# Performance work log

Hardware: AMD Instinct MI355X
Metric: run time of the kernel (lower is better)

The kernel has to match this reference:

```python
import jax, jax.numpy as jnp
import numpy as np
from jax import lax

B, S, PH, N = 4, 512, 4096, 16384
D, G, H, L, FF, GS = 1024, 128, 8, 4, 4096, 32
HD = D // H


def setup_inputs() -> dict:
    key = jax.random.key(0)
    ks = list(jax.random.split(key, 16))
    r = lambda k, sh: jax.random.normal(k, sh, jnp.float32) * 0.02
    return {
        'last_hidden': jax.random.normal(ks[0], (B, S, PH), jnp.float32),
        'current_pointcloud': jax.random.normal(ks[1], (B, N, 3), jnp.float32),
        'fp_w': r(ks[2], (D, PH)), 'fp_b': jnp.zeros((D,), jnp.float32),
        'sp_w': r(ks[3], (G * D, D)), 'sp_b': jnp.zeros((G * D,), jnp.float32),
        'pos_embed': r(ks[4], (1, G, D)),
        'ln1_w': jnp.ones((L, D), jnp.float32), 'ln1_b': jnp.zeros((L, D), jnp.float32),
        'in_w': r(ks[5], (L, 3 * D, D)), 'in_b': jnp.zeros((L, 3 * D), jnp.float32),
        'out_w': r(ks[6], (L, D, D)), 'out_b': jnp.zeros((L, D), jnp.float32),
        'ln2_w': jnp.ones((L, D), jnp.float32), 'ln2_b': jnp.zeros((L, D), jnp.float32),
        'mlp_w1': r(ks[7], (L, FF, D)), 'mlp_b1': jnp.zeros((L, FF), jnp.float32),
        'mlp_w2': r(ks[8], (L, D, FF)), 'mlp_b2': jnp.zeros((L, D), jnp.float32),
        'c1_w': r(ks[9], (D, D)), 'c1_b': jnp.zeros((D,), jnp.float32),
        'bn_g': jnp.ones((D,), jnp.float32), 'bn_beta': jnp.zeros((D,), jnp.float32),
        'bn_m': jnp.zeros((D,), jnp.float32), 'bn_v': jnp.ones((D,), jnp.float32),
        'c2_w': r(ks[10], (3 * GS, D)), 'c2_b': jnp.zeros((3 * GS,), jnp.float32),
    }


def _ln(x, w, b):
    m = jnp.mean(x, -1, keepdims=True)
    v = jnp.mean(jnp.square(x - m), -1, keepdims=True)
    return (x - m) * lax.rsqrt(v + 1e-5) * w + b


def _fps(xyz, num_samples):
    # iterative farthest point sampling; deterministic start index 0
    Bb, Nn, _ = xyz.shape
    dist0 = jnp.full((Bb, Nn), 1e10, xyz.dtype)
    far0 = jnp.zeros((Bb,), jnp.int32)

    def step(carry, _):
        dist, far = carry
        centroid = jnp.take_along_axis(xyz, far[:, None, None], axis=1)  # [B,1,3]
        d = jnp.sum(jnp.square(xyz - centroid), -1)                      # [B,N]
        dist = jnp.minimum(dist, d)
        return (dist, jnp.argmax(dist, -1).astype(jnp.int32)), far

    _, cents = lax.scan(step, (dist0, far0), None, length=num_samples)
    cents = cents.T  # [B, num_samples]
    return jnp.take_along_axis(xyz, cents[:, :, None], axis=1)  # [B,num_samples,3]


def reference(last_hidden, current_pointcloud, fp_w, fp_b, sp_w, sp_b, pos_embed,
              ln1_w, ln1_b, in_w, in_b, out_w, out_b, ln2_w, ln2_b,
              mlp_w1, mlp_b1, mlp_w2, mlp_b2,
              c1_w, c1_b, bn_g, bn_beta, bn_m, bn_v, c2_w, c2_b):
    bsz = last_hidden.shape[0]
    agg = jnp.mean(last_hidden @ fp_w.T + fp_b, axis=1)          # [B,D]
    x = (agg @ sp_w.T + sp_b).reshape(bsz, G, D)                 # [B,G,D]
    centers = _fps(current_pointcloud, G)                        # [B,G,3]
    scale = 1.0 / np.sqrt(HD).astype(np.float32)

    def block(x, p):
        l1w, l1b, iw, ib, ow, ob, l2w, l2b, w1, b1, w2, b2 = p
        xn = _ln(x + pos_embed, l1w, l1b)
        qkv = xn @ iw.T + ib                                     # [B,G,3D]
        q, k, v = jnp.split(qkv, 3, axis=-1)
        hsp = lambda t: t.reshape(bsz, G, H, HD).transpose(0, 2, 1, 3)
        q, k, v = hsp(q), hsp(k), hsp(v)
        a = jax.nn.softmax(jnp.einsum('bhqd,bhkd->bhqk', q, k) * scale, axis=-1)
        o = jnp.einsum('bhqk,bhkd->bhqd', a, v).transpose(0, 2, 1, 3).reshape(bsz, G, D)
        x = x + o @ ow.T + ob
        h = jax.nn.gelu(_ln(x, l2w, l2b) @ w1.T + b1, approximate=False)
        return x + h @ w2.T + b2, None

    x, _ = lax.scan(block, x, (ln1_w, ln1_b, in_w, in_b, out_w, out_b,
                               ln2_w, ln2_b, mlp_w1, mlp_b1, mlp_w2, mlp_b2))

    # future_predictor: 1x1 conv == per-token linear; BN in eval mode
    h = x @ c1_w.T + c1_b
    h = jax.nn.relu((h - bn_m) * lax.rsqrt(bn_v + 1e-5) * bn_g + bn_beta)
    deltas = (h @ c2_w.T + c2_b).reshape(bsz * G, GS, 3)
    pred = deltas + centers.reshape(bsz * G, 1, 3)
    return pred.reshape(bsz, G * GS, 3)
```

## Files before the change

kernel.cpp:

```cpp
#include <hip/hip_runtime.h>
#include <hip/hip_bf16.h>
#include <math.h>


typedef __bf16 bf16x8_t __attribute__((ext_vector_type(8)));
typedef float  f32x4_t  __attribute__((ext_vector_type(4)));

__device__ __forceinline__ float wredsum(float v){
#pragma unroll
  for (int o = 32; o; o >>= 1) v += __shfl_down(v, o, 64);
  return v;
}

__device__ __forceinline__ bf16x8_t pack8(float4 a, float4 b){
  bf16x8_t v;
  v[0]=(__bf16)a.x; v[1]=(__bf16)a.y; v[2]=(__bf16)a.z; v[3]=(__bf16)a.w;
  v[4]=(__bf16)b.x; v[5]=(__bf16)b.y; v[6]=(__bf16)b.z; v[7]=(__bf16)b.w;
  return v;
}

__device__ __forceinline__ void gload16(const void* g, void* l){
  __builtin_amdgcn_global_load_lds((const __attribute__((address_space(1))) unsigned int*)g,
                                   (__attribute__((address_space(3))) unsigned int*)l, 16, 0, 0);
}

__device__ __forceinline__ float wmax_f32(float m){
  m = fmaxf(m, __int_as_float(__builtin_amdgcn_ds_swizzle(__float_as_int(m), 0x041F)));
  m = fmaxf(m, __int_as_float(__builtin_amdgcn_ds_swizzle(__float_as_int(m), 0x081F)));
  m = fmaxf(m, __int_as_float(__builtin_amdgcn_ds_swizzle(__float_as_int(m), 0x101F)));
  m = fmaxf(m, __int_as_float(__builtin_amdgcn_ds_swizzle(__float_as_int(m), 0x201F)));
  m = fmaxf(m, __int_as_float(__builtin_amdgcn_ds_swizzle(__float_as_int(m), 0x401F)));
  m = fmaxf(m, __shfl_xor(m, 32, 64));
  return m;
}

__global__ __launch_bounds__(1024) void fused_front(
  const float* __restrict__ pc, float* __restrict__ centers,
  const float* __restrict__ agg, const float* __restrict__ spw,
  const float* __restrict__ spb, float* __restrict__ x,
  const float* __restrict__ inw, const float* __restrict__ outw,
  const float* __restrict__ w1, const float* __restrict__ w2,
  __bf16* __restrict__ wbf)
{
  const int bid = blockIdx.x;
  const int tid = threadIdx.x;
  if (bid < 4){
    const int b = bid;
    const int lane = tid & 63;
    const float* base = pc + (size_t)b * 16384 * 3;
    float px[16], py[16], pz[16], dist[16];
    {
      union { float4 v4[12]; float f[48]; } u;
      const float4* src = (const float4*)(base + tid * 48);
#pragma unroll
      for (int q = 0; q < 12; ++q) u.v4[q] = src[q];
#pragma unroll
      for (int j = 0; j < 16; ++j){
        px[j] = u.f[j*3]; py[j] = u.f[j*3+1]; pz[j] = u.f[j*3+2];
        dist[j] = 1e10f;
      }
    }
    __shared__ unsigned long long keyslot[128];
    __shared__ float sbc[3];
    for (int i = tid; i < 128; i += 1024) keyslot[i] = 0ULL;
    __syncthreads();
    float cx = base[0], cy = base[1], cz = base[2];
    for (int t = 0; t < 128; ++t){
      if (tid == 0){
        centers[(b*128+t)*3+0] = cx;
        centers[(b*128+t)*3+1] = cy;
        centers[(b*128+t)*3+2] = cz;
      }
      if (t == 127) break;
      float bmax = -1.0f; int bidx = 0;
#pragma unroll
      for (int j = 0; j < 16; ++j){
        float dx = __fsub_rn(px[j], cx);
        float dy = __fsub_rn(py[j], cy);
        float dz = __fsub_rn(pz[j], cz);
        float d  = __fadd_rn(__fadd_rn(__fmul_rn(dx,dx), __fmul_rn(dy,dy)), __fmul_rn(dz,dz));
        float nd = fminf(dist[j], d);
        dist[j] = nd;
        if (nd > bmax){ bmax = nd; bidx = tid*16 + j; }
      }
      const float m = wmax_f32(bmax);
      const unsigned long long cand = __ballot(bmax == m);
      const int lowlane = __ffsll((long long)cand) - 1;
      const int widx = __shfl(bidx, lowlane, 64);
      if (lane == 0){
        const unsigned long long key = ((unsigned long long)__float_as_uint(m) << 32)
                                     | (unsigned long long)(0xFFFFFFFFu - (unsigned)widx);
        atomicMax(&keyslot[t], key);
      }
      __syncthreads();
      const unsigned long long gk = keyslot[t];
      const unsigned gidx = 0xFFFFFFFFu - (unsigned)(gk & 0xFFFFFFFFu);
      if ((unsigned)tid == (gidx >> 4)){
        const int jj = gidx & 15;
#pragma unroll
        for (int q2 = 0; q2 < 16; ++q2)
          if (q2 == jj){ sbc[0] = px[q2]; sbc[1] = py[q2]; sbc[2] = pz[q2]; }
      }
      __syncthreads();
      cx = sbc[0]; cy = sbc[1]; cz = sbc[2];
    }
  } else if (bid < 1028){
    __shared__ float ag[4096];
    for (int i = tid; i < 4096; i += 1024) ag[i] = agg[i];
    __syncthreads();
    const int wv = tid >> 6, lane = tid & 63;
    const int rbase = ((bid - 4)*16 + wv)*8;
    for (int rr = 0; rr < 8; ++rr){
      const int row = rbase + rr;
      const float* wp = spw + (size_t)row*1024 + lane*4;
      const float4 w0 = *(const float4*)(wp      );
      const float4 wq1 = *(const float4*)(wp + 256);
      const float4 wq2 = *(const float4*)(wp + 512);
      const float4 wq3 = *(const float4*)(wp + 768);
      float acc[4];
#pragma unroll
      for (int bb = 0; bb < 4; ++bb){
        const float* gp = &ag[bb*1024 + lane*4];
        const float4 g0 = *(const float4*)(gp      );
        const float4 g1 = *(const float4*)(gp + 256);
        const float4 g2 = *(const float4*)(gp + 512);
        const float4 g3 = *(const float4*)(gp + 768);
        acc[bb] = w0.x*g0.x + w0.y*g0.y + w0.z*g0.z + w0.w*g0.w
                + wq1.x*g1.x + wq1.y*g1.y + wq1.z*g1.z + wq1.w*g1.w
                + wq2.x*g2.x + wq2.y*g2.y + wq2.z*g2.z + wq2.w*g2.w
                + wq3.x*g3.x + wq3.y*g3.y + wq3.z*g3.z + wq3.w*g3.w;
      }
      float a0 = wredsum(acc[0]);
      float a1 = wredsum(acc[1]);
      float a2 = wredsum(acc[2]);
      float a3 = wredsum(acc[3]);
      if (lane == 0){
        const float bias = spb[row];
        x[(size_t)0*131072 + row] = a0 + bias;
        x[(size_t)1*131072 + row] = a1 + bias;
        x[(size_t)2*131072 + row] = a2 + bias;
        x[(size_t)3*131072 + row] = a3 + bias;
      }
    }
  } else {
    const size_t t = (size_t)(bid - 1028)*1024 + tid;
    const size_t i = t*8;
    const float* src;
    if (i < 3145728)       src = inw  + i;
    else if (i < 4194304)  src = outw + (i-3145728);
    else if (i < 8388608)  src = w1   + (i-4194304);
    else                   src = w2   + (i-8388608);
    float4 a = *(const float4*)src, bq = *(const float4*)(src+4);
    *(bf16x8_t*)(wbf + i) = pack8(a, bq);
  }
}

__global__ __launch_bounds__(256) void partial_kernel(const float* __restrict__ lh,
                                                      float* __restrict__ part){
  const int ph = blockIdx.x*256 + threadIdx.x;
  const int sc = blockIdx.y, b = blockIdx.z;
  const float* p = lh + ((size_t)b*512 + sc*64)*4096 + ph;
  float s0=0,s1=0,s2=0,s3=0;
  for (int j = 0; j < 64; j += 4){
    s0 += p[(size_t)(j+0)*4096];
    s1 += p[(size_t)(j+1)*4096];
    s2 += p[(size_t)(j+2)*4096];
    s3 += p[(size_t)(j+3)*4096];
  }
  part[(size_t)(b*8+sc)*4096 + ph] = (s0+s1)+(s2+s3);
}

__global__ __launch_bounds__(256) void combine_kernel(const float* __restrict__ part,
                                                      float* __restrict__ mlh){
  const int i = blockIdx.x*256 + threadIdx.x;
  const int b = i >> 12, ph = i & 4095;
  float s = 0;
#pragma unroll
  for (int sc = 0; sc < 8; ++sc) s += part[(size_t)(b*8+sc)*4096 + ph];
  mlh[i] = s * (1.0f/512.0f);
}

__global__ __launch_bounds__(256) void agg_kernel(const float* __restrict__ mlh,
                                                  const float* __restrict__ fpw,
                                                  const float* __restrict__ fpb,
                                                  float* __restrict__ agg){
  const int o = blockIdx.x*4 + (threadIdx.x>>6);
  const int lane = threadIdx.x & 63;
  const int b = o >> 10, d = o & 1023;
  const float* mp = mlh + b*4096;
  const float* wp = fpw + (size_t)d*4096;
  float s = 0;
#pragma unroll 4
  for (int j = 0; j < 64; ++j){
    int ph = lane + j*64;
    s += mp[ph] * wp[ph];
  }
  s = wredsum(s);
  if (lane == 0) agg[o] = s + fpb[d];
}

__global__ __launch_bounds__(256) void ln_kernel(const float* __restrict__ x,
                                                 const float* __restrict__ pos,
                                                 const float* __restrict__ w,
                                                 const float* __restrict__ bb,
                                                 __bf16* __restrict__ out){
  const int tok = blockIdx.x, g = tok & 127, t = threadIdx.x;
  const int lane = t & 63, wv = t >> 6;
  const float* xr = x + (size_t)tok*1024;
  float v[4];
#pragma unroll
  for (int j = 0; j < 4; ++j){
    int d = t + j*256;
    float val = xr[d];
    if (pos) val += pos[g*1024 + d];
    v[j] = val;
  }
  __shared__ float r1[4], r2[4];
  float s = wredsum(v[0]+v[1]+v[2]+v[3]);
  if (lane == 0) r1[wv] = s;
  __syncthreads();
  const float mean = (r1[0]+r1[1]+r1[2]+r1[3]) * (1.0f/1024.0f);
  float sq = 0;
#pragma unroll
  for (int j = 0; j < 4; ++j){ float d0 = v[j]-mean; sq += d0*d0; }
  sq = wredsum(sq);
  if (lane == 0) r2[wv] = sq;
  __syncthreads();
  const float var = (r2[0]+r2[1]+r2[2]+r2[3]) * (1.0f/1024.0f);
  const float rs = rsqrtf(var + 1e-5f);
#pragma unroll
  for (int j = 0; j < 4; ++j){
    int d = t + j*256;
    out[(size_t)tok*1024 + d] = (__bf16)((v[j]-mean)*rs*w[d] + bb[d]);
  }
}

__global__ __launch_bounds__(256) void gemm_sk(
  const __bf16* __restrict__ A, const __bf16* __restrict__ W,
  float* __restrict__ parts, int M, int N, int K, int kc)
{
  __shared__ __bf16 As[128*64];
  __shared__ __bf16 Ws[128*64];
  const int n0 = blockIdx.x*128, m0 = blockIdx.y*128, z = blockIdx.z;
  const int tid = threadIdx.x;
  const int lane = tid & 63, w = tid >> 6;
  const int wm = w >> 1, wn = w & 1;
  const int lr = lane & 15, g = lane >> 4;
  const int kbeg = z*kc;
  const int c0 = tid, c1 = tid+256, c2 = tid+512, c3 = tid+768;
  const int r0 = c0>>3, r1 = c1>>3, r2 = c2>>3, r3 = c3>>3;
  const int s0 = ((c0&7) ^ (r0&7))*8, s1 = ((c1&7) ^ (r1&7))*8;
  const int s2 = ((c2&7) ^ (r2&7))*8, s3 = ((c3&7) ^ (r3&7))*8;
  const __bf16* pa0 = A + (size_t)(m0+r0)*K + kbeg + s0;
  const __bf16* pa1 = A + (size_t)(m0+r1)*K + kbeg + s1;
  const __bf16* pa2 = A + (size_t)(m0+r2)*K + kbeg + s2;
  const __bf16* pa3 = A + (size_t)(m0+r3)*K + kbeg + s3;
  const __bf16* pw0 = W + (size_t)(n0+r0)*K + kbeg + s0;
  const __bf16* pw1 = W + (size_t)(n0+r1)*K + kbeg + s1;
  const __bf16* pw2 = W + (size_t)(n0+r2)*K + kbeg + s2;
  const __bf16* pw3 = W + (size_t)(n0+r3)*K + kbeg + s3;
  f32x4_t acc[4][4] = {};
  for (int k0 = 0; k0 < kc; k0 += 64){
    __syncthreads();
    gload16(pa0 + k0, &As[c0*8]);
    gload16(pa1 + k0, &As[c1*8]);
    gload16(pa2 + k0, &As[c2*8]);
    gload16(pa3 + k0, &As[c3*8]);
    gload16(pw0 + k0, &Ws[c0*8]);
    gload16(pw1 + k0, &Ws[c1*8]);
    gload16(pw2 + k0, &Ws[c2*8]);
    gload16(pw3 + k0, &Ws[c3*8]);
    __syncthreads();
#pragma unroll
    for (int ks2 = 0; ks2 < 2; ++ks2){
      bf16x8_t af[4], bf[4];
#pragma unroll
      for (int f = 0; f < 4; ++f){
        const int ra = wm*64 + f*16 + lr;
        const int rb = wn*64 + f*16 + lr;
        const int lq = ks2*4 + g;
        af[f] = *(bf16x8_t*)&As[ra*64 + (lq ^ (ra&7))*8];
        bf[f] = *(bf16x8_t*)&Ws[rb*64 + (lq ^ (rb&7))*8];
      }
#pragma unroll
      for (int i = 0; i < 4; ++i)
#pragma unroll
        for (int j = 0; j < 4; ++j)
          acc[i][j] = __builtin_amdgcn_mfma_f32_16x16x32_bf16(af[i], bf[j], acc[i][j], 0, 0, 0);
    }
  }
  float* C = parts + (size_t)z*M*N;
#pragma unroll
  for (int i = 0; i < 4; ++i)
#pragma unroll
    for (int j = 0; j < 4; ++j)
#pragma unroll
      for (int r = 0; r < 4; ++r){
        const int row = m0 + wm*64 + i*16 + g*4 + r;
        const int col = n0 + wn*64 + j*16 + lr;
        C[(size_t)row*N + col] = acc[i][j][r];
      }
}

template<int EPI>
__global__ __launch_bounds__(256) void gemm64f(
  const __bf16* __restrict__ A, const __bf16* __restrict__ W,
  const float* __restrict__ bias, __bf16* __restrict__ C,
  int M, int N, int K)
{
  __shared__ __bf16 As[64*64];
  __shared__ __bf16 Ws[128*64];
  const int n0 = blockIdx.x*128, m0 = blockIdx.y*64;
  const int tid = threadIdx.x;
  const int lane = tid & 63, w = tid >> 6;
  const int wm = w >> 1, wn = w & 1;
  const int lr = lane & 15, g = lane >> 4;
  const int cA0 = tid, cA1 = tid+256;
  const int rA0 = cA0>>3, rA1 = cA1>>3;
  const int sA0 = ((cA0&7)^(rA0&7))*8, sA1 = ((cA1&7)^(rA1&7))*8;
  const int cW0 = tid, cW1 = tid+256, cW2 = tid+512, cW3 = tid+768;
  const int rW0 = cW0>>3, rW1 = cW1>>3, rW2 = cW2>>3, rW3 = cW3>>3;
  const int sW0 = ((cW0&7)^(rW0&7))*8, sW1 = ((cW1&7)^(rW1&7))*8;
  const int sW2 = ((cW2&7)^(rW2&7))*8, sW3 = ((cW3&7)^(rW3&7))*8;
  const __bf16* pa0 = A + (size_t)(m0+rA0)*K + sA0;
  const __bf16* pa1 = A + (size_t)(m0+rA1)*K + sA1;
  const __bf16* pw0 = W + (size_t)(n0+rW0)*K + sW0;
  const __bf16* pw1 = W + (size_t)(n0+rW1)*K + sW1;
  const __bf16* pw2 = W + (size_t)(n0+rW2)*K + sW2;
  const __bf16* pw3 = W + (size_t)(n0+rW3)*K + sW3;
  f32x4_t acc[2][4] = {};
  for (int k0 = 0; k0 < K; k0 += 64){
    __syncthreads();
    gload16(pa0 + k0, &As[cA0*8]);
    gload16(pa1 + k0, &As[cA1*8]);
    gload16(pw0 + k0, &Ws[cW0*8]);
    gload16(pw1 + k0, &Ws[cW1*8]);
    gload16(pw2 + k0, &Ws[cW2*8]);
    gload16(pw3 + k0, &Ws[cW3*8]);
    __syncthreads();
#pragma unroll
    for (int ks2 = 0; ks2 < 2; ++ks2){
      bf16x8_t af[2], bf[4];
#pragma unroll
      for (int i = 0; i < 2; ++i){
        const int ra = wm*32 + i*16 + lr;
        const int lq = ks2*4 + g;
        af[i] = *(bf16x8_t*)&As[ra*64 + (lq ^ (ra&7))*8];
      }
#pragma unroll
      for (int j = 0; j < 4; ++j){
        const int rb = wn*64 + j*16 + lr;
        const int lq = ks2*4 + g;
        bf[j] = *(bf16x8_t*)&Ws[rb*64 + (lq ^ (rb&7))*8];
      }
#pragma unroll
      for (int i = 0; i < 2; ++i)
#pragma unroll
        for (int j = 0; j < 4; ++j)
          acc[i][j] = __builtin_amdgcn_mfma_f32_16x16x32_bf16(af[i], bf[j], acc[i][j], 0, 0, 0);
    }
  }
#pragma unroll
  for (int i = 0; i < 2; ++i)
#pragma unroll
    for (int j = 0; j < 4; ++j)
#pragma unroll
      for (int r = 0; r < 4; ++r){
        const int row = m0 + wm*32 + i*16 + g*4 + r;
        const int col = n0 + wn*64 + j*16 + lr;
        float v = acc[i][j][r] + bias[col];
        if (EPI == 2) v = v * 0.5f * (1.0f + erff(v * 0.70710678118654752440f));
        C[(size_t)row*N + col] = (__bf16)v;
      }
}

template<int MODE>
__global__ __launch_bounds__(256) void comb_res_ln(const float* __restrict__ parts, int nsplit,
                                                   const float* __restrict__ bias,
                                                   const float* __restrict__ pos,
                                                   const float* __restrict__ lw,
                                                   const float* __restrict__ lb,
                                                   float* __restrict__ x,
                                                   __bf16* __restrict__ xn){
  const int tok = blockIdx.x, gi = tok & 127, t = threadIdx.x;
  const int lane = t & 63, wv = t >> 6;
  float v[4];
#pragma unroll
  for (int j = 0; j < 4; ++j){
    const int d = t + j*256;
    const size_t idx = (size_t)tok*1024 + d;
    float s = 0;
    for (int z = 0; z < nsplit; ++z) s += parts[(size_t)z*524288 + idx];
    float val = x[idx] + s + bias[d];
    x[idx] = val;
    v[j] = val;
  }
  if (MODE == 2){
#pragma unroll
    for (int j = 0; j < 4; ++j){
      const int d = t + j*256;
      xn[(size_t)tok*1024 + d] = (__bf16)v[j];
    }
    return;
  }
  float u[4];
#pragma unroll
  for (int j = 0; j < 4; ++j){
    const int d = t + j*256;
    u[j] = v[j] + (MODE == 1 ? pos[gi*1024 + d] : 0.0f);
  }
  __shared__ float r1[4], r2[4];
  float s1 = wredsum(u[0]+u[1]+u[2]+u[3]);
  if (lane == 0) r1[wv] = s1;
  __syncthreads();
  const float mean = (r1[0]+r1[1]+r1[2]+r1[3]) * (1.0f/1024.0f);
  float sq = 0;
#pragma unroll
  for (int j = 0; j < 4; ++j){ float d0 = u[j]-mean; sq += d0*d0; }
  sq = wredsum(sq);
  if (lane == 0) r2[wv] = sq;
  __syncthreads();
  const float var = (r2[0]+r2[1]+r2[2]+r2[3]) * (1.0f/1024.0f);
  const float rs = rsqrtf(var + 1e-5f);
#pragma unroll
  for (int j = 0; j < 4; ++j){
    const int d = t + j*256;
    xn[(size_t)tok*1024 + d] = (__bf16)((u[j]-mean)*rs*lw[d] + lb[d]);
  }
}

__global__ __launch_bounds__(256) void attn_fused(const __bf16* __restrict__ qkv,
                                                  __bf16* __restrict__ O,
                                                  const float* __restrict__ cs0,
                                                  const float* __restrict__ cs1,
                                                  const float* __restrict__ cs2,
                                                  const float* __restrict__ cs3,
                                                  __bf16* __restrict__ cdst,
                                                  int nch){
  if (blockIdx.x >= 64){
    const int t = (blockIdx.x - 64)*256 + threadIdx.x;
    if (t < nch){
      const size_t i = (size_t)t*8;
      const float* src;
      if (cs1 == nullptr){
        src = cs0 + i;
      } else {
        if (i < 3145728)       src = cs0 + i;
        else if (i < 4194304)  src = cs1 + (i-3145728);
        else if (i < 8388608)  src = cs2 + (i-4194304);
        else                   src = cs3 + (i-8388608);
      }
      float4 a = *(const float4*)src, bq = *(const float4*)(src+4);
      *(bf16x8_t*)(cdst + i) = pack8(a, bq);
    }
    return;
  }
  const int bh = blockIdx.x >> 1, half = blockIdx.x & 1;
  const int b = bh>>3, h = bh&7;
  const int tid = threadIdx.x, w = tid>>6, lane = tid&63;
  const int lr = lane&15, g = lane>>4;
  __shared__ __bf16 vt[128*128];
  __shared__ __bf16 pl[4*2048];
  {
    const int n = tid >> 1, kh = tid & 1;
    const __bf16* vbase = qkv + (size_t)(b*128)*3072 + 2048 + h*128 + n;
#pragma unroll
    for (int jb = 0; jb < 8; ++jb){
      bf16x8_t pk;
#pragma unroll
      for (int e = 0; e < 8; ++e) pk[e] = vbase[(size_t)(kh*64 + jb*8 + e)*3072];
      const int cb = kh*8 + jb;
      *(bf16x8_t*)&vt[n*128 + ((cb ^ (n&7)) * 8)] = pk;
    }
  }
  const __bf16* qbase = qkv + (size_t)(b*128)*3072 + h*128;
  const __bf16* kbase = qbase + 1024;
  const int qrow0 = half*64 + w*16;
  f32x4_t acc[8] = {};
#pragma unroll
  for (int ks = 0; ks < 4; ++ks){
    bf16x8_t aq, bk[8];
    aq = *(const bf16x8_t*)(qbase + (size_t)(qrow0 + lr)*3072 + ks*32 + g*8);
#pragma unroll
    for (int j = 0; j < 8; ++j)
      bk[j] = *(const bf16x8_t*)(kbase + (size_t)(j*16 + lr)*3072 + ks*32 + g*8);
#pragma unroll
    for (int j = 0; j < 8; ++j)
      acc[j] = __builtin_amdgcn_mfma_f32_16x16x32_bf16(aq, bk[j], acc[j], 0, 0, 0);
  }
  __syncthreads();
  const float scale = 0.088388347648318447f;
#pragma unroll
  for (int r = 0; r < 4; ++r){
    const int row = g*4 + r;
    float sv[8];
    float mx = -1e30f;
#pragma unroll
    for (int j = 0; j < 8; ++j){ sv[j] = acc[j][r]*scale; mx = fmaxf(mx, sv[j]); }
#pragma unroll
    for (int o = 1; o < 16; o <<= 1) mx = fmaxf(mx, __shfl_xor(mx, o, 64));
    float s = 0;
#pragma unroll
    for (int j = 0; j < 8; ++j){ sv[j] = expf(sv[j]-mx); s += sv[j]; }
#pragma unroll
    for (int o = 1; o < 16; o <<= 1) s += __shfl_xor(s, o, 64);
    const float inv = 1.0f/s;
#pragma unroll
    for (int j = 0; j < 8; ++j){
      const int col = j*16 + lr;
      const int slot = (col>>3) ^ (row&7);
      pl[w*2048 + row*128 + slot*8 + (lr&7)] = (__bf16)(sv[j]*inv);
    }
  }
  __syncthreads();
  f32x4_t acc2[8] = {};
#pragma unroll
  for (int ks = 0; ks < 4; ++ks){
    bf16x8_t ap, bv[8];
    {
      const int row = lr;
      const int slot = (ks*4 + g) ^ (row&7);
      ap = *(bf16x8_t*)&pl[w*2048 + row*128 + slot*8];
    }
#pragma unroll
    for (int j = 0; j < 8; ++j){
      const int rowv = j*16 + lr;
      const int cb = ks*4 + g;
      bv[j] = *(bf16x8_t*)&vt[rowv*128 + ((cb ^ (rowv&7))*8)];
    }
#pragma unroll
    for (int j = 0; j < 8; ++j)
      acc2[j] = __builtin_amdgcn_mfma_f32_16x16x32_bf16(ap, bv[j], acc2[j], 0, 0, 0);
  }
#pragma unroll
  for (int j = 0; j < 8; ++j)
#pragma unroll
    for (int r = 0; r < 4; ++r){
      const int row = qrow0 + g*4 + r;
      const int col = j*16 + lr;
      O[(size_t)(b*128+row)*1024 + h*128 + col] = (__bf16)acc2[j][r];
    }
}

__global__ __launch_bounds__(256) void head_kernel(const float* __restrict__ parts,
                                                   const float* __restrict__ c1b,
                                                   const float* __restrict__ bnm,
                                                   const float* __restrict__ bnv,
                                                   const float* __restrict__ bng,
                                                   const float* __restrict__ bnb,
                                                   const float* __restrict__ c2w,
                                                   const float* __restrict__ c2b,
                                                   const float* __restrict__ centers,
                                                   float* __restrict__ out){
  const int tok = blockIdx.x, t = threadIdx.x;
  const int wv = t >> 6, lane = t & 63;
  __shared__ float hrow[1024];
#pragma unroll
  for (int j = 0; j < 4; ++j){
    const int d = t + j*256;
    const size_t idx = (size_t)tok*1024 + d;
    float s = 0;
#pragma unroll
    for (int z = 0; z < 8; ++z) s += parts[(size_t)z*524288 + idx];
    float v = s + c1b[d];
    v = (v - bnm[d]) * rsqrtf(bnv[d] + 1e-5f) * bng[d] + bnb[d];
    hrow[d] = fmaxf(v, 0.0f);
  }
  __syncthreads();
  for (int i = 0; i < 24; ++i){
    const int n = wv*24 + i;
    const float* wp = c2w + (size_t)n*1024;
    float s = 0;
#pragma unroll 4
    for (int j = 0; j < 16; ++j){
      const int k = lane + j*64;
      s += hrow[k] * wp[k];
    }
    s = wredsum(s);
    if (lane == 0) out[(size_t)tok*96 + n] = s + c2b[n] + centers[tok*3 + (n % 3)];
  }
}

extern "C" void kernel_launch(void* const* d_in, const int* in_sizes, int n_in,
                              void* d_out, int out_size, void* d_ws, size_t ws_size,
                              hipStream_t stream){
  const float* lh   = (const float*)d_in[0];
  const float* pc   = (const float*)d_in[1];
  const float* fpw  = (const float*)d_in[2];
  const float* fpb  = (const float*)d_in[3];
  const float* spw  = (const float*)d_in[4];
  const float* spb  = (const float*)d_in[5];
  const float* pos  = (const float*)d_in[6];
  const float* ln1w = (const float*)d_in[7];
  const float* ln1b = (const float*)d_in[8];
  const float* inw  = (const float*)d_in[9];
  const float* inb  = (const float*)d_in[10];
  const float* outw = (const float*)d_in[11];
  const float* outb = (const float*)d_in[12];
  const float* ln2w = (const float*)d_in[13];
  const float* ln2b = (const float*)d_in[14];
  const float* w1   = (const float*)d_in[15];
  const float* b1   = (const float*)d_in[16];
  const float* w2   = (const float*)d_in[17];
  const float* b2   = (const float*)d_in[18];
  const float* c1w  = (const float*)d_in[19];
  const float* c1b  = (const float*)d_in[20];
  const float* bng  = (const float*)d_in[21];
  const float* bnbt = (const float*)d_in[22];
  const float* bnm  = (const float*)d_in[23];
  const float* bnv  = (const float*)d_in[24];
  const float* c2w  = (const float*)d_in[25];
  const float* c2b  = (const float*)d_in[26];
  float* out = (float*)d_out;

  float* f = (float*)d_ws;
  float* parts = f;              f += 16*524288;
  float* part  = f;              f += 131072;
  float* mlh   = f;              f += 16384;
  float* agg   = f;              f += 4096;
  float* x     = f;              f += 524288;
  float* cent  = f;              f += 2048;
  __bf16* bfp = (__bf16*)f;
  __bf16* xn   = bfp;            bfp += 524288;
  __bf16* qkv  = bfp;            bfp += 1572864;
  __bf16* obuf = bfp;            bfp += 524288;
  __bf16* hbf  = bfp;            bfp += 2097152;
  __bf16* xbf  = bfp;            bfp += 524288;
  __bf16* wbf  = bfp;            bfp += 51380224;

  partial_kernel<<<dim3(16,8,4), 256, 0, stream>>>(lh, part);
  combine_kernel<<<64, 256, 0, stream>>>(part, mlh);
  agg_kernel<<<1024, 256, 0, stream>>>(mlh, fpw, fpb, agg);
  fused_front<<<2564, 1024, 0, stream>>>(pc, cent, agg, spw, spb, x,
                                         inw, outw, w1, w2, wbf);
  ln_kernel<<<512, 256, 0, stream>>>(x, pos, ln1w, ln1b, xn);

  for (int l = 0; l < 4; ++l){
    const __bf16* wl = wbf + (size_t)l*12582912;
    gemm64f<0><<<dim3(24,8), 256, 0, stream>>>(xn, wl, inb + l*3072, qkv, 512, 3072, 1024);
    if (l < 3)
      attn_fused<<<64 + 6144, 256, 0, stream>>>(qkv, obuf,
          inw + (size_t)(l+1)*3145728, outw + (size_t)(l+1)*1048576,
          w1 + (size_t)(l+1)*4194304, w2 + (size_t)(l+1)*4194304,
          wbf + (size_t)(l+1)*12582912, 1572864);
    else
      attn_fused<<<64 + 512, 256, 0, stream>>>(qkv, obuf,
          c1w, nullptr, nullptr, nullptr, wbf + 50331648, 131072);
    gemm_sk<<<dim3(8,4,8), 256, 0, stream>>>(obuf, wl + 3145728, parts, 512, 1024, 1024, 128);
    comb_res_ln<0><<<512, 256, 0, stream>>>(parts, 8, outb + l*1024, nullptr,
                                            ln2w + l*1024, ln2b + l*1024, x, xn);
    gemm64f<2><<<dim3(32,8), 256, 0, stream>>>(xn, wl + 4194304, b1 + l*4096, hbf, 512, 4096, 1024);
    gemm_sk<<<dim3(8,4,8), 256, 0, stream>>>(hbf, wl + 8388608, parts, 512, 1024, 4096, 512);
    if (l < 3)
      comb_res_ln<1><<<512, 256, 0, stream>>>(parts, 8, b2 + l*1024, pos,
                                              ln1w + (l+1)*1024, ln1b + (l+1)*1024, x, xn);
    else
      comb_res_ln<2><<<512, 256, 0, stream>>>(parts, 8, b2 + l*1024, nullptr,
                                              nullptr, nullptr, x, xbf);
  }

  gemm_sk<<<dim3(8,4,8), 256, 0, stream>>>(xbf, wbf + 50331648, parts, 512, 1024, 1024, 128);
  head_kernel<<<512, 256, 0, stream>>>(parts, c1b, bnm, bnv, bng, bnbt, c2w, c2b, cent, out);
}
```

Measured before the change: 730.0 us.

## Fuse transformer layer loop into persistent megakernel with grid barriers

Replaces the per-layer sequence of roughly thirty kernel launches with a single persistent 256-block kernel that runs every stage (QKV GEMM, attention, split-K GEMMs, residual+LN, MLP, head) and separates stages with a software grid barrier built on atomics. The fp32-to-bf16 weight conversion for the next layer is spread across the idle blocks during the QKV and attention phases. The intent is to remove launch gaps and tail effects between many short kernels. In exchange, each stage is limited to 256 blocks, so attention uses only 64 blocks while the rest wait, and each barrier adds atomic spin-wait latency; correctness relies on all 256 blocks being resident at once.

After: 1.747 ms. 139% more time.

```diff
diff --git a/kernel.cpp b/kernel.cpp
--- a/kernel.cpp
+++ b/kernel.cpp
@@ -211,9 +211,7 @@
 #pragma unroll
   for (int j = 0; j < 4; ++j){
     int d = t + j*256;
-    float val = xr[d];
-    if (pos) val += pos[g*1024 + d];
-    v[j] = val;
+    v[j] = xr[d] + pos[g*1024 + d];
   }
   __shared__ float r1[4], r2[4];
   float s = wredsum(v[0]+v[1]+v[2]+v[3]);
@@ -235,13 +233,13 @@
   }
 }
 
-__global__ __launch_bounds__(256) void gemm_sk(
-  const __bf16* __restrict__ A, const __bf16* __restrict__ W,
-  float* __restrict__ parts, int M, int N, int K, int kc)
-{
-  __shared__ __bf16 As[128*64];
-  __shared__ __bf16 Ws[128*64];
-  const int n0 = blockIdx.x*128, m0 = blockIdx.y*128, z = blockIdx.z;
+
+__device__ void dev_gemm_sk(char* sm, int bx, int by, int bz,
+                            const __bf16* __restrict__ A, const __bf16* __restrict__ W,
+                            float* __restrict__ parts, int M, int N, int K, int kc){
+  __bf16* As = (__bf16*)sm;
+  __bf16* Ws = (__bf16*)(sm + 16384);
+  const int n0 = bx*128, m0 = by*128, z = bz;
   const int tid = threadIdx.x;
   const int lane = tid & 63, w = tid >> 6;
   const int wm = w >> 1, wn = w & 1;
@@ -303,14 +301,13 @@
 }
 
 template<int EPI>
-__global__ __launch_bounds__(256) void gemm64f(
-  const __bf16* __restrict__ A, const __bf16* __restrict__ W,
-  const float* __restrict__ bias, __bf16* __restrict__ C,
-  int M, int N, int K)
-{
-  __shared__ __bf16 As[64*64];
-  __shared__ __bf16 Ws[128*64];
-  const int n0 = blockIdx.x*128, m0 = blockIdx.y*64;
+__device__ void dev_gemm64f(char* sm, int bx, int by,
+                            const __bf16* __restrict__ A, const __bf16* __restrict__ W,
+                            const float* __restrict__ bias, __bf16* __restrict__ C,
+                            int N, int K){
+  __bf16* As = (__bf16*)sm;
+  __bf16* Ws = (__bf16*)(sm + 8192);
+  const int n0 = bx*128, m0 = by*64;
   const int tid = threadIdx.x;
   const int lane = tid & 63, w = tid >> 6;
   const int wm = w >> 1, wn = w & 1;
@@ -374,93 +371,15 @@
       }
 }
 
-template<int MODE>
-__global__ __launch_bounds__(256) void comb_res_ln(const float* __restrict__ parts, int nsplit,
-                                                   const float* __restrict__ bias,
-                                                   const float* __restrict__ pos,
-                                                   const float* __restrict__ lw,
-                                                   const float* __restrict__ lb,
-                                                   float* __restrict__ x,
-                                                   __bf16* __restrict__ xn){
-  const int tok = blockIdx.x, gi = tok & 127, t = threadIdx.x;
-  const int lane = t & 63, wv = t >> 6;
-  float v[4];
-#pragma unroll
-  for (int j = 0; j < 4; ++j){
-    const int d = t + j*256;
-    const size_t idx = (size_t)tok*1024 + d;
-    float s = 0;
-    for (int z = 0; z < nsplit; ++z) s += parts[(size_t)z*524288 + idx];
-    float val = x[idx] + s + bias[d];
-    x[idx] = val;
-    v[j] = val;
-  }
-  if (MODE == 2){
-#pragma unroll
-    for (int j = 0; j < 4; ++j){
-      const int d = t + j*256;
-      xn[(size_t)tok*1024 + d] = (__bf16)v[j];
-    }
-    return;
-  }
-  float u[4];
-#pragma unroll
-  for (int j = 0; j < 4; ++j){
-    const int d = t + j*256;
-    u[j] = v[j] + (MODE == 1 ? pos[gi*1024 + d] : 0.0f);
-  }
-  __shared__ float r1[4], r2[4];
-  float s1 = wredsum(u[0]+u[1]+u[2]+u[3]);
-  if (lane == 0) r1[wv] = s1;
-  __syncthreads();
-  const float mean = (r1[0]+r1[1]+r1[2]+r1[3]) * (1.0f/1024.0f);
-  float sq = 0;
-#pragma unroll
-  for (int j = 0; j < 4; ++j){ float d0 = u[j]-mean; sq += d0*d0; }
-  sq = wredsum(sq);
-  if (lane == 0) r2[wv] = sq;
-  __syncthreads();
-  const float var = (r2[0]+r2[1]+r2[2]+r2[3]) * (1.0f/1024.0f);
-  const float rs = rsqrtf(var + 1e-5f);
-#pragma unroll
-  for (int j = 0; j < 4; ++j){
-    const int d = t + j*256;
-    xn[(size_t)tok*1024 + d] = (__bf16)((u[j]-mean)*rs*lw[d] + lb[d]);
-  }
-}
-
-__global__ __launch_bounds__(256) void attn_fused(const __bf16* __restrict__ qkv,
-                                                  __bf16* __restrict__ O,
-                                                  const float* __restrict__ cs0,
-                                                  const float* __restrict__ cs1,
-                                                  const float* __restrict__ cs2,
-                                                  const float* __restrict__ cs3,
-                                                  __bf16* __restrict__ cdst,
-                                                  int nch){
-  if (blockIdx.x >= 64){
-    const int t = (blockIdx.x - 64)*256 + threadIdx.x;
-    if (t < nch){
-      const size_t i = (size_t)t*8;
-      const float* src;
-      if (cs1 == nullptr){
-        src = cs0 + i;
-      } else {
-        if (i < 3145728)       src = cs0 + i;
-        else if (i < 4194304)  src = cs1 + (i-3145728);
-        else if (i < 8388608)  src = cs2 + (i-4194304);
-        else                   src = cs3 + (i-8388608);
-      }
-      float4 a = *(const float4*)src, bq = *(const float4*)(src+4);
-      *(bf16x8_t*)(cdst + i) = pack8(a, bq);
-    }
-    return;
-  }
-  const int bh = blockIdx.x >> 1, half = blockIdx.x & 1;
+__device__ void dev_attn(char* sm, int vb,
+                         const __bf16* __restrict__ qkv, __bf16* __restrict__ O){
+  __bf16* vt = (__bf16*)sm;
+  __bf16* pl = (__bf16*)(sm + 32768);
+  const int bh = vb >> 1, half = vb & 1;
   const int b = bh>>3, h = bh&7;
   const int tid = threadIdx.x, w = tid>>6, lane = tid&63;
   const int lr = lane&15, g = lane>>4;
-  __shared__ __bf16 vt[128*128];
-  __shared__ __bf16 pl[4*2048];
+  __syncthreads();
   {
     const int n = tid >> 1, kh = tid & 1;
     const __bf16* vbase = qkv + (size_t)(b*128)*3072 + 2048 + h*128 + n;
@@ -542,19 +461,74 @@
     }
 }
 
-__global__ __launch_bounds__(256) void head_kernel(const float* __restrict__ parts,
-                                                   const float* __restrict__ c1b,
-                                                   const float* __restrict__ bnm,
-                                                   const float* __restrict__ bnv,
-                                                   const float* __restrict__ bng,
-                                                   const float* __restrict__ bnb,
-                                                   const float* __restrict__ c2w,
-                                                   const float* __restrict__ c2b,
-                                                   const float* __restrict__ centers,
-                                                   float* __restrict__ out){
-  const int tok = blockIdx.x, t = threadIdx.x;
+template<int MODE>
+__device__ void dev_comb_res_ln(char* sm, int tok,
+                                const float* __restrict__ parts,
+                                const float* __restrict__ bias,
+                                const float* __restrict__ pos,
+                                const float* __restrict__ lw,
+                                const float* __restrict__ lb,
+                                float* __restrict__ x, __bf16* __restrict__ xn){
+  float* r1 = (float*)sm;
+  float* r2 = r1 + 4;
+  const int gi = tok & 127, t = threadIdx.x;
+  const int lane = t & 63, wv = t >> 6;
+  __syncthreads();
+  float v[4];
+#pragma unroll
+  for (int j = 0; j < 4; ++j){
+    const int d = t + j*256;
+    const size_t idx = (size_t)tok*1024 + d;
+    float s = 0;
+#pragma unroll
+    for (int z = 0; z < 8; ++z) s += parts[(size_t)z*524288 + idx];
+    float val = x[idx] + s + bias[d];
+    x[idx] = val;
+    v[j] = val;
+  }
+  if (MODE == 2){
+#pragma unroll
+    for (int j = 0; j < 4; ++j){
+      const int d = t + j*256;
+      xn[(size_t)tok*1024 + d] = (__bf16)v[j];
+    }
+    return;
+  }
+  float u[4];
+#pragma unroll
+  for (int j = 0; j < 4; ++j){
+    const int d = t + j*256;
+    u[j] = v[j] + (MODE == 1 ? pos[gi*1024 + d] : 0.0f);
+  }
+  float s1 = wredsum(u[0]+u[1]+u[2]+u[3]);
+  if (lane == 0) r1[wv] = s1;
+  __syncthreads();
+  const float mean = (r1[0]+r1[1]+r1[2]+r1[3]) * (1.0f/1024.0f);
+  float sq = 0;
+#pragma unroll
+  for (int j = 0; j < 4; ++j){ float d0 = u[j]-mean; sq += d0*d0; }
+  sq = wredsum(sq);
+  if (lane == 0) r2[wv] = sq;
+  __syncthreads();
+  const float var = (r2[0]+r2[1]+r2[2]+r2[3]) * (1.0f/1024.0f);
+  const float rs = rsqrtf(var + 1e-5f);
+#pragma unroll
+  for (int j = 0; j < 4; ++j){
+    const int d = t + j*256;
+    xn[(size_t)tok*1024 + d] = (__bf16)((u[j]-mean)*rs*lw[d] + lb[d]);
+  }
+}
+
+__device__ void dev_head(char* sm, int tok,
+                         const float* __restrict__ parts, const float* __restrict__ c1b,
+                         const float* __restrict__ bnm, const float* __restrict__ bnv,
+                         const float* __restrict__ bng, const float* __restrict__ bnb,
+                         const float* __restrict__ c2w, const float* __restrict__ c2b,
+                         const float* __restrict__ centers, float* __restrict__ out){
+  float* hrow = (float*)sm;
+  const int t = threadIdx.x;
   const int wv = t >> 6, lane = t & 63;
-  __shared__ float hrow[1024];
+  __syncthreads();
 #pragma unroll
   for (int j = 0; j < 4; ++j){
     const int d = t + j*256;
@@ -579,6 +553,110 @@
     s = wredsum(s);
     if (lane == 0) out[(size_t)tok*96 + n] = s + c2b[n] + centers[tok*3 + (n % 3)];
   }
+}
+
+__device__ void dev_conv_layer(int ll, int cbase, int cstride, int cnt,
+                               const float* inw, const float* outw,
+                               const float* w1, const float* w2,
+                               __bf16* wbf){
+  for (int k = 0; k < cnt; ++k){
+    const size_t c = (size_t)cbase + (size_t)k*cstride;
+    const size_t i = c*8;
+    const float* src;
+    if (i < 3145728)       src = inw  + (size_t)ll*3145728 + i;
+    else if (i < 4194304)  src = outw + (size_t)ll*1048576 + (i-3145728);
+    else if (i < 8388608)  src = w1   + (size_t)ll*4194304 + (i-4194304);
+    else                   src = w2   + (size_t)ll*4194304 + (i-8388608);
+    float4 a = *(const float4*)src, bq = *(const float4*)(src+4);
+    *(bf16x8_t*)(wbf + (size_t)ll*12582912 + i) = pack8(a, bq);
+  }
+}
+
+__device__ __forceinline__ void gridbar(unsigned* cnt, unsigned* gen){
+  __syncthreads();
+  if (threadIdx.x == 0){
+    __threadfence();
+    const unsigned g = atomicAdd(gen, 0u);
+    const unsigned arr = atomicAdd(cnt, 1u);
+    if (arr == 255u){
+      atomicExch(cnt, 0u);
+      atomicAdd(gen, 1u);
+    } else {
+      while (atomicAdd(gen, 0u) == g){ __builtin_amdgcn_s_sleep(8); }
+    }
+    __threadfence();
+  }
+  __syncthreads();
+}
+
+struct MP {
+  const float *inw, *outw, *w1, *w2, *c1w;
+  const float *inb, *outb, *ln2w, *ln2b, *b1, *b2, *pos, *ln1w, *ln1b;
+  const float *c1b, *bnm, *bnv, *bng, *bnb, *c2w, *c2b, *cent;
+  float *parts, *x, *out;
+  __bf16 *wbf, *xn, *qkv, *obuf, *hbf, *xbf;
+  unsigned *bcnt, *bgen;
+};
+
+__global__ __launch_bounds__(256, 1) void mega(MP p){
+  __shared__ __align__(16) char smem[49152];
+  const int bid = blockIdx.x;
+  const int tid = threadIdx.x;
+  for (int l = 0; l < 4; ++l){
+    const __bf16* wl = p.wbf + (size_t)l*12582912;
+    if (bid < 192){
+      dev_gemm64f<0>(smem, bid % 24, bid / 24, p.xn, wl, p.inb + l*3072, p.qkv, 3072, 1024);
+    } else {
+      const int th = (bid-192)*256 + tid;
+      if (l < 3) dev_conv_layer(l+1, th, 16384, 24, p.inw, p.outw, p.w1, p.w2, p.wbf);
+      else {
+        for (int k = 0; k < 8; ++k){
+          const size_t i = ((size_t)th + (size_t)k*16384)*8;
+          float4 a = *(const float4*)(p.c1w + i), bq = *(const float4*)(p.c1w + i + 4);
+          *(bf16x8_t*)(p.wbf + 50331648 + i) = pack8(a, bq);
+        }
+      }
+    }
+    gridbar(p.bcnt, p.bgen);
+    if (bid < 64){
+      dev_attn(smem, bid, p.qkv, p.obuf);
+    } else if (l < 3){
+      const int th = (bid-64)*256 + tid;
+      dev_conv_layer(l+1, 393216 + th, 49152, 24, p.inw, p.outw, p.w1, p.w2, p.wbf);
+    }
+    gridbar(p.bcnt, p.bgen);
+    dev_gemm_sk(smem, bid & 7, (bid >> 3) & 3, bid >> 5,
+                p.obuf, wl + 3145728, p.parts, 512, 1024, 1024, 128);
+    gridbar(p.bcnt, p.bgen);
+    dev_comb_res_ln<0>(smem, 2*bid,   p.parts, p.outb + l*1024, nullptr,
+                       p.ln2w + l*1024, p.ln2b + l*1024, p.x, p.xn);
+    dev_comb_res_ln<0>(smem, 2*bid+1, p.parts, p.outb + l*1024, nullptr,
+                       p.ln2w + l*1024, p.ln2b + l*1024, p.x, p.xn);
+    gridbar(p.bcnt, p.bgen);
+    dev_gemm64f<2>(smem, bid & 31, bid >> 5, p.xn, wl + 4194304, p.b1 + l*4096,
+                   p.hbf, 4096, 1024);
+    gridbar(p.bcnt, p.bgen);
+    dev_gemm_sk(smem, bid & 7, (bid >> 3) & 3, bid >> 5,
+                p.hbf, wl + 8388608, p.parts, 512, 1024, 4096, 512);
+    gridbar(p.bcnt, p.bgen);
+    if (l < 3){
+      dev_comb_res_ln<1>(smem, 2*bid,   p.parts, p.b2 + l*1024, p.pos,
+                         p.ln1w + (l+1)*1024, p.ln1b + (l+1)*1024, p.x, p.xn);
+      dev_comb_res_ln<1>(smem, 2*bid+1, p.parts, p.b2 + l*1024, p.pos,
+                         p.ln1w + (l+1)*1024, p.ln1b + (l+1)*1024, p.x, p.xn);
+    } else {
+      dev_comb_res_ln<2>(smem, 2*bid,   p.parts, p.b2 + l*1024, nullptr,
+                         nullptr, nullptr, p.x, p.xbf);
+      dev_comb_res_ln<2>(smem, 2*bid+1, p.parts, p.b2 + l*1024, nullptr,
+                         nullptr, nullptr, p.x, p.xbf);
+    }
+    gridbar(p.bcnt, p.bgen);
+  }
+  dev_gemm_sk(smem, bid & 7, (bid >> 3) & 3, bid >> 5,
+              p.xbf, p.wbf + 50331648, p.parts, 512, 1024, 1024, 128);
+  gridbar(p.bcnt, p.bgen);
+  dev_head(smem, 2*bid,   p.parts, p.c1b, p.bnm, p.bnv, p.bng, p.bnb, p.c2w, p.c2b, p.cent, p.out);
+  dev_head(smem, 2*bid+1, p.parts, p.c1b, p.bnm, p.bnv, p.bng, p.bnb, p.c2w, p.c2b, p.cent, p.out);
 }
 
 extern "C" void kernel_launch(void* const* d_in, const int* in_sizes, int n_in,
@@ -620,6 +698,7 @@
   float* agg   = f;              f += 4096;
   float* x     = f;              f += 524288;
   float* cent  = f;              f += 2048;
+  unsigned* bar = (unsigned*)f;  f += 16;
   __bf16* bfp = (__bf16*)f;
   __bf16* xn   = bfp;            bfp += 524288;
   __bf16* qkv  = bfp;            bfp += 1572864;
@@ -628,6 +707,7 @@
   __bf16* xbf  = bfp;            bfp += 524288;
   __bf16* wbf  = bfp;            bfp += 51380224;
 
+  hipMemsetAsync(bar, 0, 2*sizeof(unsigned), stream);
   partial_kernel<<<dim3(16,8,4), 256, 0, stream>>>(lh, part);
   combine_kernel<<<64, 256, 0, stream>>>(part, mlh);
   agg_kernel<<<1024, 256, 0, stream>>>(mlh, fpw, fpb, agg);
@@ -635,30 +715,15 @@
                                          inw, outw, w1, w2, wbf);
   ln_kernel<<<512, 256, 0, stream>>>(x, pos, ln1w, ln1b, xn);
 
-  for (int l = 0; l < 4; ++l){
-    const __bf16* wl = wbf + (size_t)l*12582912;
-    gemm64f<0><<<dim3(24,8), 256, 0, stream>>>(xn, wl, inb + l*3072, qkv, 512, 3072, 1024);
-    if (l < 3)
-      attn_fused<<<64 + 6144, 256, 0, stream>>>(qkv, obuf,
-          inw + (size_t)(l+1)*3145728, outw + (size_t)(l+1)*1048576,
-          w1 + (size_t)(l+1)*4194304, w2 + (size_t)(l+1)*4194304,
-          wbf + (size_t)(l+1)*12582912, 1572864);
-    else
-      attn_fused<<<64 + 512, 256, 0, stream>>>(qkv, obuf,
-          c1w, nullptr, nullptr, nullptr, wbf + 50331648, 131072);
-    gemm_sk<<<dim3(8,4,8), 256, 0, stream>>>(obuf, wl + 3145728, parts, 512, 1024, 1024, 128);
-    comb_res_ln<0><<<512, 256, 0, stream>>>(parts, 8, outb + l*1024, nullptr,
-                                            ln2w + l*1024, ln2b + l*1024, x, xn);
-    gemm64f<2><<<dim3(32,8), 256, 0, stream>>>(xn, wl + 4194304, b1 + l*4096, hbf, 512, 4096, 1024);
-    gemm_sk<<<dim3(8,4,8), 256, 0, stream>>>(hbf, wl + 8388608, parts, 512, 1024, 4096, 512);
-    if (l < 3)
-      comb_res_ln<1><<<512, 256, 0, stream>>>(parts, 8, b2 + l*1024, pos,
-                                              ln1w + (l+1)*1024, ln1b + (l+1)*1024, x, xn);
-    else
-      comb_res_ln<2><<<512, 256, 0, stream>>>(parts, 8, b2 + l*1024, nullptr,
-                                              nullptr, nullptr, x, xbf);
-  }
-
-  gemm_sk<<<dim3(8,4,8), 256, 0, stream>>>(xbf, wbf + 50331648, parts, 512, 1024, 1024, 128);
-  head_kernel<<<512, 256, 0, stream>>>(parts, c1b, bnm, bnv, bng, bnbt, c2w, c2b, cent, out);
-}
+  MP mp;
+  mp.inw = inw; mp.outw = outw; mp.w1 = w1; mp.w2 = w2; mp.c1w = c1w;
+  mp.inb = inb; mp.outb = outb; mp.ln2w = ln2w; mp.ln2b = ln2b;
+  mp.b1 = b1; mp.b2 = b2; mp.pos = pos; mp.ln1w = ln1w; mp.ln1b = ln1b;
+  mp.c1b = c1b; mp.bnm = bnm; mp.bnv = bnv; mp.bng = bng; mp.bnb = bnbt;
+  mp.c2w = c2w; mp.c2b = c2b; mp.cent = cent;
+  mp.parts = parts; mp.x = x; mp.out = out;
+  mp.wbf = wbf; mp.xn = xn; mp.qkv = qkv; mp.obuf = obuf; mp.hbf = hbf; mp.xbf = xbf;
+  mp.bcnt = bar; mp.bgen = bar + 1;
+
+  mega<<<256, 256, 0, stream>>>(mp);
+}
```
